# Optimization experiments

Measured on AMD Instinct MI355X. Metric: run time of the kernel, lower is better.

The kernel has to match this reference:

```python
import jax, jax.numpy as jnp
import numpy as np

D = 1024
H = 16
HD = D // H
FF = 4 * D
EPS = 1e-5


def setup_inputs() -> dict:
    key = jax.random.key(0)
    ks = jax.random.split(key, 16)
    s = lambda k, shape, scale: jax.random.normal(k, shape, dtype=jnp.float32) * scale
    inp = {
        "x": s(ks[0], (8, 1024, D), 1.0),
        "Wq": s(ks[1], (D, D), D ** -0.5), "bq": jnp.zeros((D,), jnp.float32),
        "Wk": s(ks[2], (D, D), D ** -0.5), "bk": jnp.zeros((D,), jnp.float32),
        "Wv": s(ks[3], (D, D), D ** -0.5), "bv": jnp.zeros((D,), jnp.float32),
        "Wo": s(ks[4], (D, D), D ** -0.5), "bo": jnp.zeros((D,), jnp.float32),
        "W1": s(ks[5], (D, FF), D ** -0.5), "b1": jnp.zeros((FF,), jnp.float32),
        "W2": s(ks[6], (FF, D), FF ** -0.5), "b2": jnp.zeros((D,), jnp.float32),
        "g1": jnp.ones((D,), jnp.float32), "be1": jnp.zeros((D,), jnp.float32),
        "g2": jnp.ones((D,), jnp.float32), "be2": jnp.zeros((D,), jnp.float32),
    }
    return inp


def _layernorm(x, g, b):
    mu = jnp.mean(x, axis=-1, keepdims=True)
    var = jnp.var(x, axis=-1, keepdims=True)
    return (x - mu) * jax.lax.rsqrt(var + EPS) * g + b


def reference(x, Wq, bq, Wk, bk, Wv, bv, Wo, bo, W1, b1, W2, b2, g1, be1, g2, be2):
    B, S, _ = x.shape
    # --- pre-norm attention block (dropout = identity in eval) ---
    h = _layernorm(x, g1, be1)
    q = (h @ Wq + bq).reshape(B, S, H, HD)
    k = (h @ Wk + bk).reshape(B, S, H, HD)
    v = (h @ Wv + bv).reshape(B, S, H, HD)
    scores = jnp.einsum('bqhd,bkhd->bhqk', q, k) / jnp.sqrt(jnp.float32(HD))
    attn = jax.nn.softmax(scores, axis=-1)
    ctx = jnp.einsum('bhqk,bkhd->bqhd', attn, v).reshape(B, S, D)
    x = x + (ctx @ Wo + bo)
    # --- pre-norm FFN block ---
    h = _layernorm(x, g2, be2)
    h = jax.nn.gelu(h @ W1 + b1, approximate=False)
    x = x + (h @ W2 + b2)
    return x
```

## Files before the change

### kernel.cpp

```cpp
#include <hip/hip_runtime.h>
#include <hip/hip_bf16.h>
#include <math.h>
#include <stdint.h>

typedef unsigned short u16;
typedef unsigned int u32;
typedef __attribute__((ext_vector_type(8))) short short8;
typedef __attribute__((ext_vector_type(4))) float f32x4;

__device__ __forceinline__ float b2f(u16 u) {
  union { u32 i; float f; } v; v.i = ((u32)u) << 16; return v.f;
}
__device__ __forceinline__ u16 f2b(float f) {
  union { float f; u32 i; } v; v.f = f;
  return (u16)((v.i + 0x7FFFu + ((v.i >> 16) & 1u)) >> 16);
}

__device__ __forceinline__ void gload_lds16(const u16* g, u16* l) {
  __builtin_amdgcn_global_load_lds((const __attribute__((address_space(1))) void*)g,
                                   (__attribute__((address_space(3))) void*)l, 16, 0, 0);
}

#define LD8(p) (*(const short8*)(p))
#define MFMA_BF16 __builtin_amdgcn_mfma_f32_16x16x32_bf16

__global__ __launch_bounds__(256) void transpose_k(const float* __restrict__ in,
                                                   u16* __restrict__ out, int K, int N) {
  __shared__ u16 tile[32][33];
  int n0 = blockIdx.x * 32, k0 = blockIdx.y * 32;
  int tx = threadIdx.x & 31, ty = threadIdx.x >> 5;
  #pragma unroll
  for (int i = ty; i < 32; i += 8)
    tile[i][tx] = f2b(in[(size_t)(k0 + i) * N + n0 + tx]);
  __syncthreads();
  #pragma unroll
  for (int i = ty; i < 32; i += 8)
    out[(size_t)(n0 + i) * K + k0 + tx] = tile[tx][i];
}

__global__ __launch_bounds__(256) void cat3_k(const float* __restrict__ a, const float* __restrict__ b,
                                              const float* __restrict__ c, float* __restrict__ o) {
  int i = blockIdx.x * 256 + threadIdx.x;
  o[i] = i < 1024 ? a[i] : (i < 2048 ? b[i - 1024] : c[i - 2048]);
}

__global__ __launch_bounds__(256) void vtrans_k(const u16* __restrict__ qkv, u16* __restrict__ vt) {
  __shared__ u16 tile[32][33];
  int bh = blockIdx.y, b = bh >> 4, h = bh & 15;
  int s0 = (blockIdx.x & 31) * 32, d0 = (blockIdx.x >> 5) * 32;
  int tx = threadIdx.x & 31, ty = threadIdx.x >> 5;
  #pragma unroll
  for (int i = ty; i < 32; i += 8)
    tile[i][tx] = qkv[(size_t)(b * 1024 + s0 + i) * 3072 + 2048 + h * 64 + d0 + tx];
  __syncthreads();
  #pragma unroll
  for (int i = ty; i < 32; i += 8)
    vt[(size_t)(bh * 64 + d0 + i) * 1024 + s0 + tx] = tile[tx][i];
}

template<int FP32IN>
__global__ __launch_bounds__(256) void ln_k(const void* __restrict__ xv, const float* __restrict__ g,
                                            const float* __restrict__ be, u16* __restrict__ out) {
  int row = blockIdx.x, t = threadIdx.x;
  float f0, f1, f2, f3;
  if (FP32IN) {
    const float* xr = (const float*)xv + (size_t)row * 1024;
    float4 x4 = *(const float4*)(xr + t * 4);
    f0 = x4.x; f1 = x4.y; f2 = x4.z; f3 = x4.w;
  } else {
    const u16* xr = (const u16*)xv + (size_t)row * 1024;
    ushort4 x4 = *(const ushort4*)(xr + t * 4);
    f0 = b2f(x4.x); f1 = b2f(x4.y); f2 = b2f(x4.z); f3 = b2f(x4.w);
  }
  float s = f0 + f1 + f2 + f3;
  float ss = f0 * f0 + f1 * f1 + f2 * f2 + f3 * f3;
  #pragma unroll
  for (int off = 32; off > 0; off >>= 1) { s += __shfl_down(s, off); ss += __shfl_down(ss, off); }
  __shared__ float sb[4], ssb[4];
  if ((t & 63) == 0) { sb[t >> 6] = s; ssb[t >> 6] = ss; }
  __syncthreads();
  s = sb[0] + sb[1] + sb[2] + sb[3];
  ss = ssb[0] + ssb[1] + ssb[2] + ssb[3];
  float mu = s * (1.0f / 1024.0f);
  float var = ss * (1.0f / 1024.0f) - mu * mu;
  float rstd = rsqrtf(var + 1e-5f);
  float4 gv = *(const float4*)(g + t * 4);
  float4 bv = *(const float4*)(be + t * 4);
  ushort4 o;
  o.x = f2b((f0 - mu) * rstd * gv.x + bv.x);
  o.y = f2b((f1 - mu) * rstd * gv.y + bv.y);
  o.z = f2b((f2 - mu) * rstd * gv.z + bv.z);
  o.w = f2b((f3 - mu) * rstd * gv.w + bv.w);
  *(ushort4*)(out + (size_t)row * 1024 + t * 4) = o;
}

template<int ACT, int RESID, int OUTF32>
__global__ __launch_bounds__(256) void gemm_k(const u16* __restrict__ A, const u16* __restrict__ Bt,
                                              const float* __restrict__ bias, const void* __restrict__ resid,
                                              void* __restrict__ Cv, int M, int N, int K, int ldc) {
  __shared__ u16 As[2][128 * 32];
  __shared__ u16 Bs[2][128 * 32];
  int Ny = N >> 7;
  int lin = blockIdx.y * 64 + blockIdx.x;
  int c8 = lin & 7, sblk = lin >> 3;
  int mq = sblk / Ny;
  int m0 = ((mq << 3) | c8) << 7;
  int n0 = (sblk - mq * Ny) << 7;
  int t = threadIdx.x;
  int wave = t >> 6, lane = t & 63, quad = lane >> 4, l16 = lane & 15;
  int wm = (wave >> 1) * 64, wn = (wave & 1) * 64;
  f32x4 acc[4][4] = {};
  int lr = lane >> 2;
  int lc = (lane & 3) ^ ((lane >> 3) & 3);
  const u16* Ab = A + (size_t)(m0 + wave * 16 + lr) * K + lc * 8;
  const u16* Bb = Bt + (size_t)(n0 + wave * 16 + lr) * K + lc * 8;
  const int lb = wave * 16 * 32;
  const int rdoff = (quad ^ ((l16 >> 1) & 3)) * 8;
  #pragma unroll
  for (int i = 0; i < 2; i++) {
    gload_lds16(Ab + (size_t)i * 64 * K, &As[0][lb + i * 64 * 32]);
    gload_lds16(Bb + (size_t)i * 64 * K, &Bs[0][lb + i * 64 * 32]);
  }
  const int niter = K >> 5;
  for (int c = 0; c < niter; c++) {
    int buf = c & 1;
    __syncthreads();
    if (c + 1 < niter) {
      int k1 = (c + 1) << 5;
      #pragma unroll
      for (int i = 0; i < 2; i++) {
        gload_lds16(Ab + k1 + (size_t)i * 64 * K, &As[buf ^ 1][lb + i * 64 * 32]);
        gload_lds16(Bb + k1 + (size_t)i * 64 * K, &Bs[buf ^ 1][lb + i * 64 * 32]);
      }
    }
    short8 a[4], b[4];
    #pragma unroll
    for (int i = 0; i < 4; i++)
      a[i] = LD8(&As[buf][(wm + i * 16 + l16) * 32 + rdoff]);
    #pragma unroll
    for (int j = 0; j < 4; j++)
      b[j] = LD8(&Bs[buf][(wn + j * 16 + l16) * 32 + rdoff]);
    #pragma unroll
    for (int i = 0; i < 4; i++)
      #pragma unroll
      for (int j = 0; j < 4; j++)
        acc[i][j] = MFMA_BF16(a[i], b[j], acc[i][j], 0, 0, 0);
  }
  float bcol[4];
  #pragma unroll
  for (int j = 0; j < 4; j++) bcol[j] = bias[n0 + wn + j * 16 + l16];
  #pragma unroll
  for (int i = 0; i < 4; i++) {
    #pragma unroll
    for (int r = 0; r < 4; r++) {
      int row = m0 + wm + i * 16 + quad * 4 + r;
      #pragma unroll
      for (int j = 0; j < 4; j++) {
        int col = n0 + wn + j * 16 + l16;
        float v = acc[i][j][r] + bcol[j];
        if (ACT == 1) {
          float e = v * (2.3022082f + 0.1029431f * v * v);
          float tt = exp2f(fminf(e, 80.0f));
          v = v * tt / (tt + 1.0f);
        }
        if (RESID == 1) v += b2f(((const u16*)resid)[(size_t)row * N + col]);
        if (RESID == 2) v += ((const float*)resid)[(size_t)row * N + col];
        if (OUTF32) ((float*)Cv)[(size_t)row * ldc + col] = v;
        else        ((u16*)Cv)[(size_t)row * ldc + col] = f2b(v);
      }
    }
  }
}

template<int ACT, int RESID, int OUTF32>
__global__ __launch_bounds__(512, 2) void gemm256_k(const u16* __restrict__ A, const u16* __restrict__ Bt,
                                                    const float* __restrict__ bias, const void* __restrict__ resid,
                                                    void* __restrict__ Cv, int M, int N, int K, int ldc) {
  __shared__ u16 As[4][256 * 32];
  __shared__ u16 Bs[4][256 * 32];
  int Ny = N >> 8;
  int lin = blockIdx.y * 32 + blockIdx.x;
  int c8 = lin & 7, sblk = lin >> 3;
  int mq = sblk / Ny;
  int m0 = ((mq << 3) | c8) << 8;
  int n0 = (sblk - mq * Ny) << 8;
  int t = threadIdx.x;
  int wave = t >> 6, lane = t & 63, quad = lane >> 4, l16 = lane & 15;
  int wm = (wave >> 2) << 7;
  int wn = (wave & 3) << 6;
  f32x4 acc[8][4] = {};
  int lr = lane >> 2;
  int lc = (lane & 3) ^ ((lane >> 3) & 3);
  const u16* Ab = A + (size_t)(m0 + wave * 16 + lr) * K + lc * 8;
  const u16* Bb = Bt + (size_t)(n0 + wave * 16 + lr) * K + lc * 8;
  const int lbA = wave * 16 * 32;
  const int cswz = (quad ^ ((l16 >> 1) & 3)) * 8;
  const int rdA = (wm + l16) * 32 + cswz;
  const int rdB = (wn + l16) * 32 + cswz;
  const int niter = K >> 5;
  #pragma unroll
  for (int p = 0; p < 3; p++) {
    #pragma unroll
    for (int g = 0; g < 2; g++) {
      gload_lds16(Ab + (p << 5) + (size_t)g * 128 * K, &As[p][lbA + g * 128 * 32]);
      gload_lds16(Bb + (p << 5) + (size_t)g * 128 * K, &Bs[p][lbA + g * 128 * 32]);
    }
  }
  asm volatile("s_waitcnt vmcnt(8)" ::: "memory");
  __builtin_amdgcn_s_barrier();
  __builtin_amdgcn_sched_barrier(0);
  for (int tt = 0; tt < niter; tt++) {
    int buf = tt & 3, wb = (tt + 3) & 3;
    const bool pf = (tt + 3 < niter);
    const int kpf = (tt + 3) << 5;
    const u16* Ac = &As[buf][0];
    const u16* Bc = &Bs[buf][0];
    short8 a[8], b[4];
    a[0] = LD8(Ac + rdA);
    a[1] = LD8(Ac + rdA + 512);
    a[2] = LD8(Ac + rdA + 1024);
    a[3] = LD8(Ac + rdA + 1536);
    b[0] = LD8(Bc + rdB);
    b[1] = LD8(Bc + rdB + 512);
    b[2] = LD8(Bc + rdB + 1024);
    b[3] = LD8(Bc + rdB + 1536);
    if (pf) {
      gload_lds16(Ab + kpf, &As[wb][lbA]);
      gload_lds16(Ab + kpf + (size_t)128 * K, &As[wb][lbA + 128 * 32]);
    }
    __builtin_amdgcn_s_barrier();
    asm volatile("s_waitcnt lgkmcnt(0)" ::: "memory");
    __builtin_amdgcn_sched_barrier(0);
    __builtin_amdgcn_s_setprio(1);
    #pragma unroll
    for (int i = 0; i < 4; i++)
      #pragma unroll
      for (int j = 0; j < 4; j++)
        acc[i][j] = MFMA_BF16(a[i], b[j], acc[i][j], 0, 0, 0);
    __builtin_amdgcn_s_setprio(0);
    __builtin_amdgcn_s_barrier();
    __builtin_amdgcn_sched_barrier(0);
    a[4] = LD8(Ac + rdA + 2048);
    a[5] = LD8(Ac + rdA + 2560);
    a[6] = LD8(Ac + rdA + 3072);
    a[7] = LD8(Ac + rdA + 3584);
    if (pf) {
      gload_lds16(Bb + kpf, &Bs[wb][lbA]);
      gload_lds16(Bb + kpf + (size_t)128 * K, &Bs[wb][lbA + 128 * 32]);
    }
    __builtin_amdgcn_s_barrier();
    asm volatile("s_waitcnt lgkmcnt(0)" ::: "memory");
    __builtin_amdgcn_sched_barrier(0);
    __builtin_amdgcn_s_setprio(1);
    #pragma unroll
    for (int i = 4; i < 8; i++)
      #pragma unroll
      for (int j = 0; j < 4; j++)
        acc[i][j] = MFMA_BF16(a[i], b[j], acc[i][j], 0, 0, 0);
    __builtin_amdgcn_s_setprio(0);
    if (tt + 3 < niter) {
      asm volatile("s_waitcnt vmcnt(8)" ::: "memory");
    } else if (tt + 2 < niter) {
      asm volatile("s_waitcnt vmcnt(4)" ::: "memory");
    } else if (tt + 1 < niter) {
      asm volatile("s_waitcnt vmcnt(0)" ::: "memory");
    }
    if (tt + 1 < niter) {
      __builtin_amdgcn_s_barrier();
      __builtin_amdgcn_sched_barrier(0);
    }
  }
  float bcol[4];
  #pragma unroll
  for (int j = 0; j < 4; j++) bcol[j] = bias[n0 + wn + j * 16 + l16];
  #pragma unroll
  for (int i = 0; i < 8; i++) {
    #pragma unroll
    for (int r = 0; r < 4; r++) {
      int row = m0 + wm + i * 16 + quad * 4 + r;
      #pragma unroll
      for (int j = 0; j < 4; j++) {
        int col = n0 + wn + j * 16 + l16;
        float v = acc[i][j][r] + bcol[j];
        if (ACT == 1) {
          float e = v * (2.3022082f + 0.1029431f * v * v);
          float tt2 = exp2f(fminf(e, 80.0f));
          v = v * tt2 / (tt2 + 1.0f);
        }
        if (RESID == 1) v += b2f(((const u16*)resid)[(size_t)row * N + col]);
        if (RESID == 2) v += ((const float*)resid)[(size_t)row * N + col];
        if (OUTF32) ((float*)Cv)[(size_t)row * ldc + col] = v;
        else        ((u16*)Cv)[(size_t)row * ldc + col] = f2b(v);
      }
    }
  }
}

__global__ __launch_bounds__(256) void attn_k(const u16* __restrict__ QKV, const u16* __restrict__ VT,
                                              u16* __restrict__ ctx) {
  int bh = blockIdx.x;
  int b = bh >> 4;
  int q0 = blockIdx.y * 64;
  int t = threadIdx.x, wave = t >> 6, lane = t & 63, quad = lane >> 4, l16 = lane & 15;
  __shared__ u16 Ks[2][64 * 64];
  __shared__ u16 Vs[2][64 * 64];
  __shared__ u16 Plds[4][16][72];
  const size_t base = ((size_t)b * 1024) * 3072 + (size_t)(bh & 15) * 64;
  const u16* Kbase = QKV + base + 1024;
  const u16* vtb = VT + (size_t)bh * 64 * 1024;
  int lrow = lane >> 3;
  int lchunk = (lane & 7) ^ (lrow & 7);
  int srow = wave * 16;
  short8 qa[2];
  #pragma unroll
  for (int kh = 0; kh < 2; kh++)
    qa[kh] = *(const short8*)(QKV + base + (size_t)(q0 + wave * 16 + l16) * 3072 + kh * 32 + quad * 8);
  #pragma unroll
  for (int half = 0; half < 2; half++) {
    int r8 = srow + half * 8;
    gload_lds16(Kbase + (size_t)(r8 + lrow) * 3072 + lchunk * 8, &Ks[0][r8 * 64]);
    gload_lds16(vtb + (size_t)(r8 + lrow) * 1024 + lchunk * 8, &Vs[0][r8 * 64]);
  }
  f32x4 o[4] = {};
  float l_acc[4] = {0.f, 0.f, 0.f, 0.f};
  for (int c = 0; c < 16; c++) {
    int buf = c & 1;
    __syncthreads();
    if (c < 15) {
      #pragma unroll
      for (int half = 0; half < 2; half++) {
        int r8 = srow + half * 8;
        gload_lds16(Kbase + (size_t)((c + 1) * 64 + r8 + lrow) * 3072 + lchunk * 8, &Ks[buf ^ 1][r8 * 64]);
        gload_lds16(vtb + (size_t)(r8 + lrow) * 1024 + (c + 1) * 64 + lchunk * 8, &Vs[buf ^ 1][r8 * 64]);
      }
    }
    f32x4 s[4] = {};
    #pragma unroll
    for (int kh = 0; kh < 2; kh++)
      #pragma unroll
      for (int j = 0; j < 4; j++) {
        int row = j * 16 + l16;
        int pc = (kh * 4 + quad) ^ (row & 7);
        short8 kb = *(const short8*)(&Ks[buf][row * 64 + pc * 8]);
        s[j] = MFMA_BF16(qa[kh], kb, s[j], 0, 0, 0);
      }
    #pragma unroll
    for (int j = 0; j < 4; j++)
      #pragma unroll
      for (int r = 0; r < 4; r++) {
        float p = exp2f(s[j][r] * 0.18033688011112042f);
        l_acc[r] += p;
        Plds[wave][quad * 4 + r][j * 16 + l16] = f2b(p);
      }
    #pragma unroll
    for (int kh = 0; kh < 2; kh++) {
      short8 pa = *(const short8*)(&Plds[wave][l16][kh * 32 + quad * 8]);
      #pragma unroll
      for (int d4 = 0; d4 < 4; d4++) {
        int row = d4 * 16 + l16;
        int pc = (kh * 4 + quad) ^ (row & 7);
        short8 vb = *(const short8*)(&Vs[buf][row * 64 + pc * 8]);
        o[d4] = MFMA_BF16(pa, vb, o[d4], 0, 0, 0);
      }
    }
  }
  #pragma unroll
  for (int off = 1; off < 16; off <<= 1)
    #pragma unroll
    for (int r = 0; r < 4; r++) l_acc[r] += __shfl_xor(l_acc[r], off);
  #pragma unroll
  for (int r = 0; r < 4; r++) {
    float inv = 1.0f / l_acc[r];
    size_t row = (size_t)b * 1024 + q0 + wave * 16 + quad * 4 + r;
    #pragma unroll
    for (int d4 = 0; d4 < 4; d4++) {
      int col = (bh & 15) * 64 + d4 * 16 + l16;
      ctx[row * 1024 + col] = f2b(o[d4][r] * inv);
    }
  }
}

extern "C" void kernel_launch(void* const* d_in, const int* in_sizes, int n_in,
                              void* d_out, int out_size, void* d_ws, size_t ws_size,
                              hipStream_t stream) {
  const float* x   = (const float*)d_in[0];
  const float* Wq  = (const float*)d_in[1];  const float* bq  = (const float*)d_in[2];
  const float* Wk  = (const float*)d_in[3];  const float* bk  = (const float*)d_in[4];
  const float* Wv  = (const float*)d_in[5];  const float* bv  = (const float*)d_in[6];
  const float* Wo  = (const float*)d_in[7];  const float* bo  = (const float*)d_in[8];
  const float* W1  = (const float*)d_in[9];  const float* b1  = (const float*)d_in[10];
  const float* W2  = (const float*)d_in[11]; const float* b2  = (const float*)d_in[12];
  const float* g1  = (const float*)d_in[13]; const float* be1 = (const float*)d_in[14];
  const float* g2  = (const float*)d_in[15]; const float* be2 = (const float*)d_in[16];

  char* ws = (char*)d_ws;
  const size_t MB = 1024 * 1024;
  u16* h1    = (u16*)(ws + 0 * MB);
  u16* qkv   = (u16*)(ws + 16 * MB);
  u16* x1    = (u16*)(ws + 16 * MB);
  u16* h2    = (u16*)(ws + 32 * MB);
  u16* W2T   = (u16*)(ws + 48 * MB);
  u16* WqkvT = (u16*)(ws + 64 * MB);
  u16* WoT   = (u16*)(ws + 70 * MB);
  u16* W1T   = (u16*)(ws + 72 * MB);
  float* bqkv = (float*)(ws + 80 * MB);
  u16* h3f   = (u16*)(ws + 80 * MB);
  u16* vt    = h1;
  u16* ctx   = (u16*)d_out;
  float* out = (float*)d_out;

  transpose_k<<<dim3(32, 32), 256, 0, stream>>>(Wq, WqkvT, 1024, 1024);
  transpose_k<<<dim3(32, 32), 256, 0, stream>>>(Wk, WqkvT + (size_t)1024 * 1024, 1024, 1024);
  transpose_k<<<dim3(32, 32), 256, 0, stream>>>(Wv, WqkvT + (size_t)2048 * 1024, 1024, 1024);
  transpose_k<<<dim3(32, 32), 256, 0, stream>>>(Wo, WoT, 1024, 1024);
  transpose_k<<<dim3(128, 32), 256, 0, stream>>>(W1, W1T, 1024, 4096);
  cat3_k<<<12, 256, 0, stream>>>(bq, bk, bv, bqkv);

  ln_k<1><<<8192, 256, 0, stream>>>(x, g1, be1, h1);

  gemm256_k<0, 0, 0><<<dim3(32, 12), 512, 0, stream>>>(h1, WqkvT, bqkv, nullptr, qkv,
                                                       8192, 3072, 1024, 3072);

  vtrans_k<<<dim3(64, 128), 256, 0, stream>>>(qkv, vt);

  attn_k<<<dim3(128, 16), 256, 0, stream>>>(qkv, vt, ctx);

  gemm_k<0, 2, 0><<<dim3(64, 8), 256, 0, stream>>>(ctx, WoT, bo, x, x1,
                                                   8192, 1024, 1024, 1024);

  transpose_k<<<dim3(32, 128), 256, 0, stream>>>(W2, W2T, 4096, 1024);

  ln_k<0><<<8192, 256, 0, stream>>>(x1, g2, be2, h2);

  gemm256_k<1, 0, 0><<<dim3(32, 16), 512, 0, stream>>>(h2, W1T, b1, nullptr, h3f,
                                                       8192, 4096, 1024, 4096);
  gemm_k<0, 1, 1><<<dim3(64, 8), 256, 0, stream>>>(h3f, W2T, b2, x1, out,
                                                   8192, 1024, 4096, 1024);

  (void)in_sizes; (void)n_in; (void)out_size; (void)ws_size;
}
```

Before: 545.8 us.

## Restructure 256x256 GEMM to double-buffered BK=64 tiles with XOR swizzle

```diff
diff --git a/kernel.cpp b/kernel.cpp
--- a/kernel.cpp
+++ b/kernel.cpp
@@ -176,8 +176,8 @@
 __global__ __launch_bounds__(512, 2) void gemm256_k(const u16* __restrict__ A, const u16* __restrict__ Bt,
                                                     const float* __restrict__ bias, const void* __restrict__ resid,
                                                     void* __restrict__ Cv, int M, int N, int K, int ldc) {
-  __shared__ u16 As[4][256 * 32];
-  __shared__ u16 Bs[4][256 * 32];
+  __shared__ u16 As[2][256 * 64];
+  __shared__ u16 Bs[2][256 * 64];
   int Ny = N >> 8;
   int lin = blockIdx.y * 32 + blockIdx.x;
   int c8 = lin & 7, sblk = lin >> 3;
@@ -189,83 +189,160 @@
   int wm = (wave >> 2) << 7;
   int wn = (wave & 3) << 6;
   f32x4 acc[8][4] = {};
-  int lr = lane >> 2;
-  int lc = (lane & 3) ^ ((lane >> 3) & 3);
-  const u16* Ab = A + (size_t)(m0 + wave * 16 + lr) * K + lc * 8;
-  const u16* Bb = Bt + (size_t)(n0 + wave * 16 + lr) * K + lc * 8;
-  const int lbA = wave * 16 * 32;
-  const int cswz = (quad ^ ((l16 >> 1) & 3)) * 8;
-  const int rdA = (wm + l16) * 32 + cswz;
-  const int rdB = (wn + l16) * 32 + cswz;
-  const int niter = K >> 5;
-  #pragma unroll
-  for (int p = 0; p < 3; p++) {
-    #pragma unroll
-    for (int g = 0; g < 2; g++) {
-      gload_lds16(Ab + (p << 5) + (size_t)g * 128 * K, &As[p][lbA + g * 128 * 32]);
-      gload_lds16(Bb + (p << 5) + (size_t)g * 128 * K, &Bs[p][lbA + g * 128 * 32]);
-    }
-  }
-  asm volatile("s_waitcnt vmcnt(8)" ::: "memory");
+  int lrow = lane >> 3;
+  int lchunk = (lane & 7) ^ lrow;
+  const u16* Ab = A + (size_t)(m0 + wave * 32 + lrow) * K + lchunk * 8;
+  const u16* Bb = Bt + (size_t)(n0 + wave * 32 + lrow) * K + lchunk * 8;
+  const int sbase = wave * 32 * 64;
+  const int x7 = l16 & 7;
+  const int rdA = (wm + l16) * 64;
+  const int rdB = (wn + l16) * 64;
+  const int cz0 = (quad ^ x7) * 8;
+  const int cz1 = ((4 + quad) ^ x7) * 8;
+  const int niter = K >> 6;
+  #pragma unroll
+  for (int g = 0; g < 4; g++) {
+    gload_lds16(Ab + (size_t)g * 8 * K, &As[0][sbase + g * 8 * 64]);
+    gload_lds16(Bb + (size_t)g * 8 * K, &Bs[0][sbase + g * 8 * 64]);
+  }
+  asm volatile("s_waitcnt vmcnt(0)" ::: "memory");
   __builtin_amdgcn_s_barrier();
   __builtin_amdgcn_sched_barrier(0);
   for (int tt = 0; tt < niter; tt++) {
-    int buf = tt & 3, wb = (tt + 3) & 3;
-    const bool pf = (tt + 3 < niter);
-    const int kpf = (tt + 3) << 5;
+    int buf = tt & 1;
+    const bool pf = (tt + 1 < niter);
+    const int kpf = (tt + 1) << 6;
     const u16* Ac = &As[buf][0];
     const u16* Bc = &Bs[buf][0];
-    short8 a[8], b[4];
-    a[0] = LD8(Ac + rdA);
-    a[1] = LD8(Ac + rdA + 512);
-    a[2] = LD8(Ac + rdA + 1024);
-    a[3] = LD8(Ac + rdA + 1536);
-    b[0] = LD8(Bc + rdB);
-    b[1] = LD8(Bc + rdB + 512);
-    b[2] = LD8(Bc + rdB + 1024);
-    b[3] = LD8(Bc + rdB + 1536);
+    u16* Aw = &As[buf ^ 1][0];
+    u16* Bw = &Bs[buf ^ 1][0];
+    short8 a0, a1, a2, a3, a4, a5, a6, a7, b0, b1, b2, b3;
+    a0 = LD8(Ac + rdA + cz0);
+    a1 = LD8(Ac + rdA + 1024 + cz0);
+    a2 = LD8(Ac + rdA + 2048 + cz0);
+    a3 = LD8(Ac + rdA + 3072 + cz0);
+    b0 = LD8(Bc + rdB + cz0);
+    b1 = LD8(Bc + rdB + 1024 + cz0);
+    b2 = LD8(Bc + rdB + 2048 + cz0);
+    b3 = LD8(Bc + rdB + 3072 + cz0);
     if (pf) {
-      gload_lds16(Ab + kpf, &As[wb][lbA]);
-      gload_lds16(Ab + kpf + (size_t)128 * K, &As[wb][lbA + 128 * 32]);
+      #pragma unroll
+      for (int g = 0; g < 4; g++)
+        gload_lds16(Ab + kpf + (size_t)g * 8 * K, Aw + sbase + g * 8 * 64);
     }
     __builtin_amdgcn_s_barrier();
     asm volatile("s_waitcnt lgkmcnt(0)" ::: "memory");
     __builtin_amdgcn_sched_barrier(0);
     __builtin_amdgcn_s_setprio(1);
-    #pragma unroll
-    for (int i = 0; i < 4; i++)
-      #pragma unroll
-      for (int j = 0; j < 4; j++)
-        acc[i][j] = MFMA_BF16(a[i], b[j], acc[i][j], 0, 0, 0);
+    acc[0][0] = MFMA_BF16(a0, b0, acc[0][0], 0, 0, 0);
+    acc[0][1] = MFMA_BF16(a0, b1, acc[0][1], 0, 0, 0);
+    acc[0][2] = MFMA_BF16(a0, b2, acc[0][2], 0, 0, 0);
+    acc[0][3] = MFMA_BF16(a0, b3, acc[0][3], 0, 0, 0);
+    acc[1][0] = MFMA_BF16(a1, b0, acc[1][0], 0, 0, 0);
+    acc[1][1] = MFMA_BF16(a1, b1, acc[1][1], 0, 0, 0);
+    acc[1][2] = MFMA_BF16(a1, b2, acc[1][2], 0, 0, 0);
+    acc[1][3] = MFMA_BF16(a1, b3, acc[1][3], 0, 0, 0);
+    acc[2][0] = MFMA_BF16(a2, b0, acc[2][0], 0, 0, 0);
+    acc[2][1] = MFMA_BF16(a2, b1, acc[2][1], 0, 0, 0);
+    acc[2][2] = MFMA_BF16(a2, b2, acc[2][2], 0, 0, 0);
+    acc[2][3] = MFMA_BF16(a2, b3, acc[2][3], 0, 0, 0);
+    acc[3][0] = MFMA_BF16(a3, b0, acc[3][0], 0, 0, 0);
+    acc[3][1] = MFMA_BF16(a3, b1, acc[3][1], 0, 0, 0);
+    acc[3][2] = MFMA_BF16(a3, b2, acc[3][2], 0, 0, 0);
+    acc[3][3] = MFMA_BF16(a3, b3, acc[3][3], 0, 0, 0);
     __builtin_amdgcn_s_setprio(0);
     __builtin_amdgcn_s_barrier();
     __builtin_amdgcn_sched_barrier(0);
-    a[4] = LD8(Ac + rdA + 2048);
-    a[5] = LD8(Ac + rdA + 2560);
-    a[6] = LD8(Ac + rdA + 3072);
-    a[7] = LD8(Ac + rdA + 3584);
+    a4 = LD8(Ac + rdA + 4096 + cz0);
+    a5 = LD8(Ac + rdA + 5120 + cz0);
+    a6 = LD8(Ac + rdA + 6144 + cz0);
+    a7 = LD8(Ac + rdA + 7168 + cz0);
     if (pf) {
-      gload_lds16(Bb + kpf, &Bs[wb][lbA]);
-      gload_lds16(Bb + kpf + (size_t)128 * K, &Bs[wb][lbA + 128 * 32]);
+      #pragma unroll
+      for (int g = 0; g < 4; g++)
+        gload_lds16(Bb + kpf + (size_t)g * 8 * K, Bw + sbase + g * 8 * 64);
     }
     __builtin_amdgcn_s_barrier();
     asm volatile("s_waitcnt lgkmcnt(0)" ::: "memory");
     __builtin_amdgcn_sched_barrier(0);
     __builtin_amdgcn_s_setprio(1);
-    #pragma unroll
-    for (int i = 4; i < 8; i++)
-      #pragma unroll
-      for (int j = 0; j < 4; j++)
-        acc[i][j] = MFMA_BF16(a[i], b[j], acc[i][j], 0, 0, 0);
+    acc[4][0] = MFMA_BF16(a4, b0, acc[4][0], 0, 0, 0);
+    acc[4][1] = MFMA_BF16(a4, b1, acc[4][1], 0, 0, 0);
+    acc[4][2] = MFMA_BF16(a4, b2, acc[4][2], 0, 0, 0);
+    acc[4][3] = MFMA_BF16(a4, b3, acc[4][3], 0, 0, 0);
+    acc[5][0] = MFMA_BF16(a5, b0, acc[5][0], 0, 0, 0);
+    acc[5][1] = MFMA_BF16(a5, b1, acc[5][1], 0, 0, 0);
+    acc[5][2] = MFMA_BF16(a5, b2, acc[5][2], 0, 0, 0);
+    acc[5][3] = MFMA_BF16(a5, b3, acc[5][3], 0, 0, 0);
+    acc[6][0] = MFMA_BF16(a6, b0, acc[6][0], 0, 0, 0);
+    acc[6][1] = MFMA_BF16(a6, b1, acc[6][1], 0, 0, 0);
+    acc[6][2] = MFMA_BF16(a6, b2, acc[6][2], 0, 0, 0);
+    acc[6][3] = MFMA_BF16(a6, b3, acc[6][3], 0, 0, 0);
+    acc[7][0] = MFMA_BF16(a7, b0, acc[7][0], 0, 0, 0);
+    acc[7][1] = MFMA_BF16(a7, b1, acc[7][1], 0, 0, 0);
+    acc[7][2] = MFMA_BF16(a7, b2, acc[7][2], 0, 0, 0);
+    acc[7][3] = MFMA_BF16(a7, b3, acc[7][3], 0, 0, 0);
     __builtin_amdgcn_s_setprio(0);
-    if (tt + 3 < niter) {
-      asm volatile("s_waitcnt vmcnt(8)" ::: "memory");
-    } else if (tt + 2 < niter) {
-      asm volatile("s_waitcnt vmcnt(4)" ::: "memory");
-    } else if (tt + 1 < niter) {
+    __builtin_amdgcn_s_barrier();
+    __builtin_amdgcn_sched_barrier(0);
+    a0 = LD8(Ac + rdA + cz1);
+    a1 = LD8(Ac + rdA + 1024 + cz1);
+    a2 = LD8(Ac + rdA + 2048 + cz1);
+    a3 = LD8(Ac + rdA + 3072 + cz1);
+    b0 = LD8(Bc + rdB + cz1);
+    b1 = LD8(Bc + rdB + 1024 + cz1);
+    b2 = LD8(Bc + rdB + 2048 + cz1);
+    b3 = LD8(Bc + rdB + 3072 + cz1);
+    __builtin_amdgcn_s_barrier();
+    asm volatile("s_waitcnt lgkmcnt(0)" ::: "memory");
+    __builtin_amdgcn_sched_barrier(0);
+    __builtin_amdgcn_s_setprio(1);
+    acc[0][0] = MFMA_BF16(a0, b0, acc[0][0], 0, 0, 0);
+    acc[0][1] = MFMA_BF16(a0, b1, acc[0][1], 0, 0, 0);
+    acc[0][2] = MFMA_BF16(a0, b2, acc[0][2], 0, 0, 0);
+    acc[0][3] = MFMA_BF16(a0, b3, acc[0][3], 0, 0, 0);
+    acc[1][0] = MFMA_BF16(a1, b0, acc[1][0], 0, 0, 0);
+    acc[1][1] = MFMA_BF16(a1, b1, acc[1][1], 0, 0, 0);
+    acc[1][2] = MFMA_BF16(a1, b2, acc[1][2], 0, 0, 0);
+    acc[1][3] = MFMA_BF16(a1, b3, acc[1][3], 0, 0, 0);
+    acc[2][0] = MFMA_BF16(a2, b0, acc[2][0], 0, 0, 0);
+    acc[2][1] = MFMA_BF16(a2, b1, acc[2][1], 0, 0, 0);
+    acc[2][2] = MFMA_BF16(a2, b2, acc[2][2], 0, 0, 0);
+    acc[2][3] = MFMA_BF16(a2, b3, acc[2][3], 0, 0, 0);
+    acc[3][0] = MFMA_BF16(a3, b0, acc[3][0], 0, 0, 0);
+    acc[3][1] = MFMA_BF16(a3, b1, acc[3][1], 0, 0, 0);
+    acc[3][2] = MFMA_BF16(a3, b2, acc[3][2], 0, 0, 0);
+    acc[3][3] = MFMA_BF16(a3, b3, acc[3][3], 0, 0, 0);
+    __builtin_amdgcn_s_setprio(0);
+    __builtin_amdgcn_s_barrier();
+    __builtin_amdgcn_sched_barrier(0);
+    a4 = LD8(Ac + rdA + 4096 + cz1);
+    a5 = LD8(Ac + rdA + 5120 + cz1);
+    a6 = LD8(Ac + rdA + 6144 + cz1);
+    a7 = LD8(Ac + rdA + 7168 + cz1);
+    __builtin_amdgcn_s_barrier();
+    asm volatile("s_waitcnt lgkmcnt(0)" ::: "memory");
+    __builtin_amdgcn_sched_barrier(0);
+    __builtin_amdgcn_s_setprio(1);
+    acc[4][0] = MFMA_BF16(a4, b0, acc[4][0], 0, 0, 0);
+    acc[4][1] = MFMA_BF16(a4, b1, acc[4][1], 0, 0, 0);
+    acc[4][2] = MFMA_BF16(a4, b2, acc[4][2], 0, 0, 0);
+    acc[4][3] = MFMA_BF16(a4, b3, acc[4][3], 0, 0, 0);
+    acc[5][0] = MFMA_BF16(a5, b0, acc[5][0], 0, 0, 0);
+    acc[5][1] = MFMA_BF16(a5, b1, acc[5][1], 0, 0, 0);
+    acc[5][2] = MFMA_BF16(a5, b2, acc[5][2], 0, 0, 0);
+    acc[5][3] = MFMA_BF16(a5, b3, acc[5][3], 0, 0, 0);
+    acc[6][0] = MFMA_BF16(a6, b0, acc[6][0], 0, 0, 0);
+    acc[6][1] = MFMA_BF16(a6, b1, acc[6][1], 0, 0, 0);
+    acc[6][2] = MFMA_BF16(a6, b2, acc[6][2], 0, 0, 0);
+    acc[6][3] = MFMA_BF16(a6, b3, acc[6][3], 0, 0, 0);
+    acc[7][0] = MFMA_BF16(a7, b0, acc[7][0], 0, 0, 0);
+    acc[7][1] = MFMA_BF16(a7, b1, acc[7][1], 0, 0, 0);
+    acc[7][2] = MFMA_BF16(a7, b2, acc[7][2], 0, 0, 0);
+    acc[7][3] = MFMA_BF16(a7, b3, acc[7][3], 0, 0, 0);
+    __builtin_amdgcn_s_setprio(0);
+    if (pf) {
       asm volatile("s_waitcnt vmcnt(0)" ::: "memory");
-    }
-    if (tt + 1 < niter) {
       __builtin_amdgcn_s_barrier();
       __builtin_amdgcn_sched_barrier(0);
     }
```

Result: no change. 537.0 us (-1.6%).
